# Performance work log

Hardware: AMD Instinct MI355X
Metric: run time of the kernel (lower is better)

Reference implementation:

```python
import jax, jax.numpy as jnp
import numpy as np

N = 8192          # num_relations
IN_DIM = 512      # 2 * entity_dim
HID = 256         # hidden_dim
REL_DIM = 256     # relation_dim


def setup_inputs() -> dict:
    key = jax.random.key(0)
    ks = jax.random.split(key, 8)
    s = 1.0 / np.sqrt(IN_DIM)
    return {
        "relation": jax.random.normal(ks[0], (N, REL_DIM), dtype=jnp.float32),
        "context": jax.random.normal(ks[1], (N, IN_DIM), dtype=jnp.float32),
        "adj_tensor": jax.random.randint(ks[2], (N, N), 0, 2).astype(jnp.float32),
        "W_common": jax.random.normal(ks[3], (HID, IN_DIM), dtype=jnp.float32) * s,
        "w_left": jax.random.normal(ks[4], (HID,), dtype=jnp.float32) * (1.0 / np.sqrt(HID)),
        "b_left": jax.random.normal(ks[5], (), dtype=jnp.float32) * 0.01,
        "w_right": jax.random.normal(ks[6], (HID,), dtype=jnp.float32) * (1.0 / np.sqrt(HID)),
        "b_right": jax.random.normal(ks[7], (), dtype=jnp.float32) * 0.01,
    }


def reference(relation, context, adj_tensor, W_common, w_left, b_left, w_right, b_right):
    # common linear (no bias): (N, IN_DIM) @ (IN_DIM, HID) -> (N, HID)
    in_fts = context @ W_common.T
    left = in_fts @ w_left + b_left          # (N,)
    right = in_fts @ w_right + b_right       # (N,)
    logits = left[:, None] + right[None, :]  # additive outer-sum -> (N, N)
    logits = jnp.where(logits >= 0, logits, 0.2 * logits)  # leaky_relu(0.2)
    logits = jnp.where(adj_tensor <= 0.0, -jnp.inf, logits)
    coefs = jax.nn.softmax(logits, axis=-1)  # (N, N)
    x = coefs @ relation                     # (N, REL_DIM)
    return jax.nn.relu(x)
```

## Files before the change

kernel.cpp:

```cpp
#include <hip/hip_runtime.h>

#define NREL 8192
#define RD   256

typedef float f32x4 __attribute__((ext_vector_type(4)));
typedef short s16x8 __attribute__((ext_vector_type(8)));
typedef unsigned int  u32;
typedef unsigned short u16;
typedef unsigned long long u64;
typedef u32 u32x4 __attribute__((ext_vector_type(4)));

__device__ __forceinline__ u16 f2bf(float f) {
    u32 b = __float_as_uint(f);
    return (u16)((b + 0x7FFFu + ((b >> 16) & 1u)) >> 16);
}
__device__ __forceinline__ u32 pk_bf16(float lo, float hi) {
    u32 r;
    asm("v_cvt_pk_bf16_f32 %0, %1, %2" : "=v"(r) : "v"(lo), "v"(hi));
    return r;
}

__global__ __launch_bounds__(256) void k_prep(
    const float* __restrict__ W, const float* __restrict__ wl,
    const float* __restrict__ wr, float* __restrict__ ul,
    float* __restrict__ ur)
{
    __shared__ float sL[256], sR[256];
    const int t = threadIdx.x;
    const int d = blockIdx.x * 16 + (t & 15);
    float aL = 0.f, aR = 0.f;
    for (int h = (t >> 4); h < 256; h += 16) {
        float w = W[h * 512 + d];
        aL += w * wl[h];
        aR += w * wr[h];
    }
    sL[t] = aL; sR[t] = aR;
    __syncthreads();
    if (t < 16) {
        float xL = 0.f, xR = 0.f;
        for (int g = 0; g < 16; g++) { xL += sL[g * 16 + t]; xR += sR[g * 16 + t]; }
        ul[blockIdx.x * 16 + t] = xL;
        ur[blockIdx.x * 16 + t] = xR;
    }
}

__global__ __launch_bounds__(256) void k_lr(
    const float* __restrict__ ctx, const float* __restrict__ ul,
    const float* __restrict__ ur, const float* __restrict__ bl,
    const float* __restrict__ br, float* __restrict__ left,
    float* __restrict__ right)
{
    const int lane = threadIdx.x & 63;
    const int row  = blockIdx.x * 4 + (threadIdx.x >> 6);
    const f32x4* cv = (const f32x4*)(ctx + (size_t)row * 512);
    const f32x4* uv = (const f32x4*)ul;
    const f32x4* vv = (const f32x4*)ur;
    f32x4 c0 = cv[lane], c1 = cv[lane + 64];
    f32x4 u0 = uv[lane], u1 = uv[lane + 64];
    f32x4 v0 = vv[lane], v1 = vv[lane + 64];
    float dl = c0.x*u0.x + c0.y*u0.y + c0.z*u0.z + c0.w*u0.w
             + c1.x*u1.x + c1.y*u1.y + c1.z*u1.z + c1.w*u1.w;
    float dr = c0.x*v0.x + c0.y*v0.y + c0.z*v0.z + c0.w*v0.w
             + c1.x*v1.x + c1.y*v1.y + c1.z*v1.z + c1.w*v1.w;
    #pragma unroll
    for (int o = 1; o < 64; o <<= 1) { dl += __shfl_xor(dl, o); dr += __shfl_xor(dr, o); }
    if (lane == 0) {
        left[row]  = dl + bl[0];
        right[row] = dr + br[0];
    }
}

__global__ __launch_bounds__(256) void k_rmax(const float* __restrict__ right,
                                              u32* __restrict__ rmaxk)
{
    __shared__ float sm[4];
    const int t = threadIdx.x;
    const f32x4* rv = (const f32x4*)right;
    float m = -3.4e38f;
    #pragma unroll
    for (int i = 0; i < 8; i++) {
        f32x4 v = rv[t + 256 * i];
        m = fmaxf(m, fmaxf(fmaxf(v.x, v.y), fmaxf(v.z, v.w)));
    }
    #pragma unroll
    for (int o = 1; o < 64; o <<= 1) m = fmaxf(m, __shfl_xor(m, o));
    if ((t & 63) == 0) sm[t >> 6] = m;
    __syncthreads();
    if (t == 0) {
        m = fmaxf(fmaxf(sm[0], sm[1]), fmaxf(sm[2], sm[3]));
        u32 b = __float_as_uint(m);
        *rmaxk = ((int)b >= 0) ? (b | 0x80000000u) : ~b;
    }
}

__global__ __launch_bounds__(256) void k_bf(const float* __restrict__ R,
                                            u32* __restrict__ Bf)
{
    const int b     = blockIdx.x;
    const int jt    = b >> 1;
    const int fbase = (b & 1) * 1024;
    #pragma unroll
    for (int rep = 0; rep < 4; rep++) {
        const int f    = fbase + rep * 256 + threadIdx.x;
        const int kk   = f >> 10;
        const int cg   = (f >> 6) & 15;
        const int lane = f & 63;
        const int lq   = lane >> 4;
        const int l15  = lane & 15;
        const int j0   = (jt << 6) + kk * 32 + lq * 8;
        const int n    = cg * 16 + l15;
        const float* src = R + (size_t)j0 * RD + n;
        float v[8];
        #pragma unroll
        for (int e = 0; e < 8; e++) v[e] = src[(size_t)e * RD];
        u32x4 w;
        w.x = pk_bf16(v[0], v[1]);
        w.y = pk_bf16(v[2], v[3]);
        w.z = pk_bf16(v[4], v[5]);
        w.w = pk_bf16(v[6], v[7]);
        *(u32x4*)(Bf + ((size_t)jt * 2048 + f) * 4) = w;
    }
}

template<int S>
__global__ __launch_bounds__(512) void k_attn_f(
    const float* __restrict__ adj, const s16x8* __restrict__ Bf,
    const float* __restrict__ left, const float* __restrict__ right,
    const u32* __restrict__ rmaxk, float* __restrict__ pnum,
    float* __restrict__ pden)
{
    __shared__ u32 Pl[2][2048];

    const int tid  = threadIdx.x;
    const int lane = tid & 63;
    const int wv   = tid >> 6;
    const int l15  = lane & 15;
    const int lq   = lane >> 4;
    const int s      = (int)(blockIdx.x % (unsigned)S);
    const int rowblk = (int)(blockIdx.x / (unsigned)S) * 64;
    const int jt0 = s * (128 / S);
    const int jt1 = jt0 + (128 / S);

    const int pr = tid >> 4;
    const int pq = tid & 15;

    const float lft0 = left[rowblk + pr];
    const float lft1 = left[rowblk + pr + 32];
    const u32 kbits = *rmaxk;
    const float rmax = __uint_as_float((kbits & 0x80000000u) ? (kbits ^ 0x80000000u)
                                                             : ~kbits);
    float z;
    z = lft0 + rmax; const float m0 = fmaxf(z, 0.2f * z);
    z = lft1 + rmax; const float m1 = fmaxf(z, 0.2f * z);

    f32x4 acc[4][2];
    #pragma unroll
    for (int i = 0; i < 4; i++) { acc[i][0] = (f32x4)0.f; acc[i][1] = (f32x4)0.f; }
    float dp0 = 0.f, dp1 = 0.f;

    const f32x4* adjv = (const f32x4*)adj;
    const f32x4* rv4  = (const f32x4*)right;
    const size_t arow0 = (size_t)(rowblk + pr) * 2048;
    const size_t arow1 = (size_t)(rowblk + pr + 32) * 2048;

    const u32 widx0 = (u32)pr * 32 + (((u32)pq * 2) ^ (((u32)pr & 7) << 2));
    const u32 widx1 = widx0 + 1024;

    f32x4 a0 = adjv[arow0 + jt0 * 16 + pq];
    f32x4 a1 = adjv[arow1 + jt0 * 16 + pq];
    f32x4 rv = rv4[jt0 * 16 + pq];
    s16x8 bcur[2][2];
    #pragma unroll
    for (int kk = 0; kk < 2; kk++)
        #pragma unroll
        for (int ct = 0; ct < 2; ct++)
            bcur[kk][ct] = Bf[(size_t)jt0 * 2048 + kk * 1024 + (wv * 2 + ct) * 64 + lane];

    int p = 0;
    for (int jt = jt0; jt < jt1; ++jt, p ^= 1) {
        float pa[4], pb[4];
        #pragma unroll
        for (int e = 0; e < 4; e++) {
            const float r = rv[e];
            float z0 = lft0 + r; float s0 = fmaxf(z0, 0.2f * z0);
            float e0 = __expf(s0 - m0);
            pa[e] = (a0[e] > 0.5f) ? e0 : 0.f;
            float z1 = lft1 + r; float s1 = fmaxf(z1, 0.2f * z1);
            float e1 = __expf(s1 - m1);
            pb[e] = (a1[e] > 0.5f) ? e1 : 0.f;
        }
        dp0 += pa[0] + pa[1] + pa[2] + pa[3];
        dp1 += pb[0] + pb[1] + pb[2] + pb[3];
        u32* Pb = Pl[p];
        Pb[widx0]     = pk_bf16(pa[0], pa[1]);
        Pb[widx0 + 1] = pk_bf16(pa[2], pa[3]);
        Pb[widx1]     = pk_bf16(pb[0], pb[1]);
        Pb[widx1 + 1] = pk_bf16(pb[2], pb[3]);

        asm volatile("s_waitcnt lgkmcnt(0)" ::: "memory");
        __builtin_amdgcn_s_barrier();

        const int jn = (jt + 1 < jt1) ? jt + 1 : jt0;
        f32x4 na0 = adjv[arow0 + jn * 16 + pq];
        f32x4 na1 = adjv[arow1 + jn * 16 + pq];
        f32x4 nrv = rv4[jn * 16 + pq];
        s16x8 bnxt[2][2];
        #pragma unroll
        for (int kk = 0; kk < 2; kk++)
            #pragma unroll
            for (int ct = 0; ct < 2; ct++)
                bnxt[kk][ct] = Bf[(size_t)jn * 2048 + kk * 1024 + (wv * 2 + ct) * 64 + lane];

        const u16* Pu = (const u16*)Pl[p];
        #pragma unroll
        for (int kk = 0; kk < 2; kk++) {
            s16x8 af[4];
            #pragma unroll
            for (int rt = 0; rt < 4; rt++) {
                const int row = rt * 16 + l15;
                const int us  = row * 64 + ((kk * 32 + lq * 8) ^ ((row & 7) << 3));
                af[rt] = *(const s16x8*)(Pu + us);
            }
            #pragma unroll
            for (int ct = 0; ct < 2; ct++)
                #pragma unroll
                for (int rt = 0; rt < 4; rt++)
                    acc[rt][ct] = __builtin_amdgcn_mfma_f32_16x16x32_bf16(
                        af[rt], bcur[kk][ct], acc[rt][ct], 0, 0, 0);
        }

        a0 = na0; a1 = na1; rv = nrv;
        #pragma unroll
        for (int kk = 0; kk < 2; kk++)
            #pragma unroll
            for (int ct = 0; ct < 2; ct++) bcur[kk][ct] = bnxt[kk][ct];
    }

    #pragma unroll
    for (int o = 1; o < 16; o <<= 1) { dp0 += __shfl_xor(dp0, o); dp1 += __shfl_xor(dp1, o); }
    if (pq == 0) {
        pden[(size_t)s * NREL + rowblk + pr]      = dp0;
        pden[(size_t)s * NREL + rowblk + pr + 32] = dp1;
    }
    float* pn = pnum + (size_t)s * NREL * RD;
    #pragma unroll
    for (int rt = 0; rt < 4; rt++)
        #pragma unroll
        for (int ct = 0; ct < 2; ct++)
            #pragma unroll
            for (int r = 0; r < 4; r++) {
                const int row = rt * 16 + lq * 4 + r;
                pn[(size_t)(rowblk + row) * RD + (wv * 32 + ct * 16 + l15)] =
                    acc[rt][ct][r];
            }
}

template<int S>
__global__ __launch_bounds__(256) void k_red(
    const float* __restrict__ pnum, const float* __restrict__ pden,
    float* __restrict__ out)
{
    const int idx = blockIdx.x * 256 + threadIdx.x;
    const int row = idx >> 6;
    float den = 0.f;
    #pragma unroll
    for (int s = 0; s < S; s++) den += pden[(size_t)s * NREL + row];
    const f32x4* pn4 = (const f32x4*)pnum;
    f32x4 a = (f32x4)0.f;
    #pragma unroll
    for (int s = 0; s < S; s++) a += pn4[(size_t)s * (NREL * RD / 4) + idx];
    f32x4 r;
    r.x = fmaxf(a.x / den, 0.f);
    r.y = fmaxf(a.y / den, 0.f);
    r.z = fmaxf(a.z / den, 0.f);
    r.w = fmaxf(a.w / den, 0.f);
    ((f32x4*)out)[idx] = r;
}

__global__ __launch_bounds__(512) void k_attn_leg(
    const float* __restrict__ adj, const float* __restrict__ rel,
    const float* __restrict__ left, const float* __restrict__ right,
    const u32* __restrict__ rmaxk, float* __restrict__ outp)
{
    __shared__ u32   Pl[64 * 32];
    __shared__ float dnm[64];
    const int tid  = threadIdx.x;
    const int lane = tid & 63;
    const int wv   = tid >> 6;
    const int l15  = lane & 15;
    const int lq   = lane >> 4;
    const int rowblk = blockIdx.x * 64;
    const int pr = tid >> 4, pq = tid & 15;
    const float lft0 = left[rowblk + pr];
    const float lft1 = left[rowblk + pr + 32];
    const u32 kbits = *rmaxk;
    const float rmax = __uint_as_float((kbits & 0x80000000u) ? (kbits ^ 0x80000000u)
                                                             : ~kbits);
    float z;
    z = lft0 + rmax; const float m0 = fmaxf(z, 0.2f * z);
    z = lft1 + rmax; const float m1 = fmaxf(z, 0.2f * z);
    f32x4 acc[4][2];
    #pragma unroll
    for (int i = 0; i < 4; i++) { acc[i][0] = (f32x4)0.f; acc[i][1] = (f32x4)0.f; }
    float dp0 = 0.f, dp1 = 0.f;
    const f32x4* adjv = (const f32x4*)adj;
    const f32x4* rv4  = (const f32x4*)right;
    const size_t arow0 = (size_t)(rowblk + pr) * 2048;
    const size_t arow1 = (size_t)(rowblk + pr + 32) * 2048;
    const int n0 = wv * 32 + l15;
    const u32 widx0 = (u32)pr * 32 + (((u32)pq * 2) ^ (((u32)pr & 7) << 2));
    const u32 widx1 = widx0 + 1024;
    for (int jb = 0; jb < NREL; jb += 64) {
        f32x4 a0 = adjv[arow0 + (jb >> 2) + pq];
        f32x4 a1 = adjv[arow1 + (jb >> 2) + pq];
        f32x4 rv = rv4[(jb >> 2) + pq];
        s16x8 bc[2][2];
        #pragma unroll
        for (int kk = 0; kk < 2; kk++)
            #pragma unroll
            for (int ct = 0; ct < 2; ct++) {
                const float* rp = rel + (size_t)(jb + kk * 32 + lq * 8) * RD
                                      + (n0 + ct * 16);
                s16x8 b;
                #pragma unroll
                for (int e = 0; e < 8; e++) b[e] = (short)f2bf(rp[(size_t)e * RD]);
                bc[kk][ct] = b;
            }
        float pa[4], pb[4];
        #pragma unroll
        for (int e = 0; e < 4; e++) {
            const float r = rv[e];
            float z0 = lft0 + r; float s0 = fmaxf(z0, 0.2f * z0);
            pa[e] = a0[e] * __expf(s0 - m0);
            float z1 = lft1 + r; float s1 = fmaxf(z1, 0.2f * z1);
            pb[e] = a1[e] * __expf(s1 - m1);
        }
        dp0 += pa[0] + pa[1] + pa[2] + pa[3];
        dp1 += pb[0] + pb[1] + pb[2] + pb[3];
        Pl[widx0]     = pk_bf16(pa[0], pa[1]);
        Pl[widx0 + 1] = pk_bf16(pa[2], pa[3]);
        Pl[widx1]     = pk_bf16(pb[0], pb[1]);
        Pl[widx1 + 1] = pk_bf16(pb[2], pb[3]);
        __syncthreads();
        #pragma unroll
        for (int kk = 0; kk < 2; kk++) {
            s16x8 af[4];
            #pragma unroll
            for (int rt = 0; rt < 4; rt++) {
                const int row = rt * 16 + l15;
                const int us  = row * 64 + ((kk * 32 + lq * 8) ^ ((row & 7) << 3));
                af[rt] = *(const s16x8*)((const u16*)Pl + us);
            }
            #pragma unroll
            for (int ct = 0; ct < 2; ct++)
                #pragma unroll
                for (int rt = 0; rt < 4; rt++)
                    acc[rt][ct] = __builtin_amdgcn_mfma_f32_16x16x32_bf16(
                        af[rt], bc[kk][ct], acc[rt][ct], 0, 0, 0);
        }
        __syncthreads();
    }
    #pragma unroll
    for (int o = 1; o < 16; o <<= 1) { dp0 += __shfl_xor(dp0, o); dp1 += __shfl_xor(dp1, o); }
    if (pq == 0) { dnm[pr] = dp0; dnm[pr + 32] = dp1; }
    __syncthreads();
    #pragma unroll
    for (int rt = 0; rt < 4; rt++)
        #pragma unroll
        for (int ct = 0; ct < 2; ct++)
            #pragma unroll
            for (int r = 0; r < 4; r++) {
                const int row = rt * 16 + lq * 4 + r;
                float v = acc[rt][ct][r] / dnm[row];
                outp[(size_t)(rowblk + row) * RD + (wv * 32 + ct * 16 + l15)] =
                    fmaxf(v, 0.f);
            }
}

extern "C" void kernel_launch(void* const* d_in, const int* in_sizes, int n_in,
                              void* d_out, int out_size, void* d_ws, size_t ws_size,
                              hipStream_t stream)
{
    const float* relation = (const float*)d_in[0];
    const float* context  = (const float*)d_in[1];
    const float* adj      = (const float*)d_in[2];
    const float* W        = (const float*)d_in[3];
    const float* wl       = (const float*)d_in[4];
    const float* bl       = (const float*)d_in[5];
    const float* wr       = (const float*)d_in[6];
    const float* br       = (const float*)d_in[7];
    float* out = (float*)d_out;

    float* wsf   = (float*)d_ws;
    float* ul    = wsf;
    float* ur    = wsf + 512;
    float* left  = wsf + 1024;
    float* right = wsf + 1024 + 8192;
    u32*   rmaxk = (u32*)(wsf + 1024 + 16384);
    const size_t hdr  = 81920;
    const size_t bf_b = (size_t)NREL * RD * 2;
    u32* Bf   = (u32*)((char*)d_ws + hdr);
    float* pnum = (float*)((char*)d_ws + hdr + bf_b);

    hipLaunchKernelGGL(k_prep, dim3(32), dim3(256), 0, stream, W, wl, wr, ul, ur);
    hipLaunchKernelGGL(k_lr, dim3(2048), dim3(256), 0, stream,
                       context, ul, ur, bl, br, left, right);
    hipLaunchKernelGGL(k_rmax, dim3(1), dim3(256), 0, stream, right, rmaxk);

    const int S = 4;
    const size_t need = hdr + bf_b
                      + (size_t)S * NREL * RD * 4 + (size_t)S * NREL * 4;

    if (ws_size >= need) {
        float* pden = pnum + (size_t)S * NREL * RD;
        hipLaunchKernelGGL(k_bf, dim3(256), dim3(256), 0, stream, relation, Bf);
        hipLaunchKernelGGL((k_attn_f<4>), dim3(128 * 4), dim3(512), 0, stream,
                           adj, (const s16x8*)Bf, left, right, rmaxk, pnum, pden);
        hipLaunchKernelGGL((k_red<4>), dim3(2048), dim3(256), 0, stream,
                           pnum, pden, out);
    } else {
        hipLaunchKernelGGL(k_attn_leg, dim3(128), dim3(512), 0, stream,
                           adj, relation, left, right, rmaxk, out);
    }
}
```

Measured before the change: 115.9 us.

## Fuse split-K reduction into attention kernel, merge prep with bf16 pack, unroll loop

Folds the relation bf16 packing into the prep kernel launch, and removes the separate split-K reduce kernel: the last of the S blocks for each row block (found via an atomic counter zeroed in k_rmax) sums the partials, normalizes and applies relu. The main loop is also manually unrolled by two with fixed LDS buffers and explicit A/B register sets. This removes two kernel launches and a pass over partial sums. In exchange it adds atomics, fences and a serialized tail on the last block of each row group.

```diff
diff --git a/kernel.cpp b/kernel.cpp
--- a/kernel.cpp
+++ b/kernel.cpp
@@ -20,27 +20,55 @@
     return r;
 }
 
-__global__ __launch_bounds__(256) void k_prep(
+__global__ __launch_bounds__(256) void k_prep_bf(
     const float* __restrict__ W, const float* __restrict__ wl,
     const float* __restrict__ wr, float* __restrict__ ul,
-    float* __restrict__ ur)
+    float* __restrict__ ur, const float* __restrict__ R,
+    u32* __restrict__ Bf)
 {
     __shared__ float sL[256], sR[256];
     const int t = threadIdx.x;
-    const int d = blockIdx.x * 16 + (t & 15);
-    float aL = 0.f, aR = 0.f;
-    for (int h = (t >> 4); h < 256; h += 16) {
-        float w = W[h * 512 + d];
-        aL += w * wl[h];
-        aR += w * wr[h];
-    }
-    sL[t] = aL; sR[t] = aR;
-    __syncthreads();
-    if (t < 16) {
-        float xL = 0.f, xR = 0.f;
-        for (int g = 0; g < 16; g++) { xL += sL[g * 16 + t]; xR += sR[g * 16 + t]; }
-        ul[blockIdx.x * 16 + t] = xL;
-        ur[blockIdx.x * 16 + t] = xR;
+    if (blockIdx.x < 32) {
+        const int d = blockIdx.x * 16 + (t & 15);
+        float aL = 0.f, aR = 0.f;
+        for (int h = (t >> 4); h < 256; h += 16) {
+            float w = W[h * 512 + d];
+            aL += w * wl[h];
+            aR += w * wr[h];
+        }
+        sL[t] = aL; sR[t] = aR;
+        __syncthreads();
+        if (t < 16) {
+            float xL = 0.f, xR = 0.f;
+            for (int g = 0; g < 16; g++) { xL += sL[g * 16 + t]; xR += sR[g * 16 + t]; }
+            ul[blockIdx.x * 16 + t] = xL;
+            ur[blockIdx.x * 16 + t] = xR;
+        }
+        return;
+    }
+    const int b     = blockIdx.x - 32;
+    const int jt    = b >> 1;
+    const int fbase = (b & 1) * 1024;
+    #pragma unroll
+    for (int rep = 0; rep < 4; rep++) {
+        const int f    = fbase + rep * 256 + t;
+        const int kk   = f >> 10;
+        const int cg   = (f >> 6) & 15;
+        const int lane = f & 63;
+        const int lq   = lane >> 4;
+        const int l15  = lane & 15;
+        const int j0   = (jt << 6) + kk * 32 + lq * 8;
+        const int n    = cg * 16 + l15;
+        const float* src = R + (size_t)j0 * RD + n;
+        float v[8];
+        #pragma unroll
+        for (int e = 0; e < 8; e++) v[e] = src[(size_t)e * RD];
+        u32x4 w;
+        w.x = pk_bf16(v[0], v[1]);
+        w.y = pk_bf16(v[2], v[3]);
+        w.z = pk_bf16(v[4], v[5]);
+        w.w = pk_bf16(v[6], v[7]);
+        *(u32x4*)(Bf + ((size_t)jt * 2048 + f) * 4) = w;
     }
 }
 
@@ -71,10 +99,12 @@
 }
 
 __global__ __launch_bounds__(256) void k_rmax(const float* __restrict__ right,
-                                              u32* __restrict__ rmaxk)
+                                              u32* __restrict__ rmaxk,
+                                              u32* __restrict__ cnt)
 {
     __shared__ float sm[4];
     const int t = threadIdx.x;
+    if (t < 128) cnt[t] = 0;
     const f32x4* rv = (const f32x4*)right;
     float m = -3.4e38f;
     #pragma unroll
@@ -93,43 +123,17 @@
     }
 }
 
-__global__ __launch_bounds__(256) void k_bf(const float* __restrict__ R,
-                                            u32* __restrict__ Bf)
-{
-    const int b     = blockIdx.x;
-    const int jt    = b >> 1;
-    const int fbase = (b & 1) * 1024;
-    #pragma unroll
-    for (int rep = 0; rep < 4; rep++) {
-        const int f    = fbase + rep * 256 + threadIdx.x;
-        const int kk   = f >> 10;
-        const int cg   = (f >> 6) & 15;
-        const int lane = f & 63;
-        const int lq   = lane >> 4;
-        const int l15  = lane & 15;
-        const int j0   = (jt << 6) + kk * 32 + lq * 8;
-        const int n    = cg * 16 + l15;
-        const float* src = R + (size_t)j0 * RD + n;
-        float v[8];
-        #pragma unroll
-        for (int e = 0; e < 8; e++) v[e] = src[(size_t)e * RD];
-        u32x4 w;
-        w.x = pk_bf16(v[0], v[1]);
-        w.y = pk_bf16(v[2], v[3]);
-        w.z = pk_bf16(v[4], v[5]);
-        w.w = pk_bf16(v[6], v[7]);
-        *(u32x4*)(Bf + ((size_t)jt * 2048 + f) * 4) = w;
-    }
-}
-
 template<int S>
 __global__ __launch_bounds__(512) void k_attn_f(
     const float* __restrict__ adj, const s16x8* __restrict__ Bf,
     const float* __restrict__ left, const float* __restrict__ right,
     const u32* __restrict__ rmaxk, float* __restrict__ pnum,
-    float* __restrict__ pden)
-{
-    __shared__ u32 Pl[2][2048];
+    float* __restrict__ pden, u32* __restrict__ cnt,
+    float* __restrict__ out)
+{
+    __shared__ u32   Pl[2][2048];
+    __shared__ float dnm[64];
+    __shared__ u32   sLast;
 
     const int tid  = threadIdx.x;
     const int lane = tid & 63;
@@ -137,7 +141,8 @@
     const int l15  = lane & 15;
     const int lq   = lane >> 4;
     const int s      = (int)(blockIdx.x % (unsigned)S);
-    const int rowblk = (int)(blockIdx.x / (unsigned)S) * 64;
+    const int rb     = (int)(blockIdx.x / (unsigned)S);
+    const int rowblk = rb * 64;
     const int jt0 = s * (128 / S);
     const int jt1 = jt0 + (128 / S);
 
@@ -166,74 +171,123 @@
     const u32 widx0 = (u32)pr * 32 + (((u32)pq * 2) ^ (((u32)pr & 7) << 2));
     const u32 widx1 = widx0 + 1024;
 
-    f32x4 a0 = adjv[arow0 + jt0 * 16 + pq];
-    f32x4 a1 = adjv[arow1 + jt0 * 16 + pq];
-    f32x4 rv = rv4[jt0 * 16 + pq];
-    s16x8 bcur[2][2];
+    f32x4 aA0 = adjv[arow0 + jt0 * 16 + pq];
+    f32x4 aA1 = adjv[arow1 + jt0 * 16 + pq];
+    f32x4 rvA = rv4[jt0 * 16 + pq];
+    f32x4 aB0 = adjv[arow0 + (jt0 + 1) * 16 + pq];
+    f32x4 aB1 = adjv[arow1 + (jt0 + 1) * 16 + pq];
+    f32x4 rvB = rv4[(jt0 + 1) * 16 + pq];
+    s16x8 bA[2][2], bB[2][2];
     #pragma unroll
     for (int kk = 0; kk < 2; kk++)
         #pragma unroll
         for (int ct = 0; ct < 2; ct++)
-            bcur[kk][ct] = Bf[(size_t)jt0 * 2048 + kk * 1024 + (wv * 2 + ct) * 64 + lane];
-
-    int p = 0;
-    for (int jt = jt0; jt < jt1; ++jt, p ^= 1) {
-        float pa[4], pb[4];
-        #pragma unroll
-        for (int e = 0; e < 4; e++) {
-            const float r = rv[e];
-            float z0 = lft0 + r; float s0 = fmaxf(z0, 0.2f * z0);
-            float e0 = __expf(s0 - m0);
-            pa[e] = (a0[e] > 0.5f) ? e0 : 0.f;
-            float z1 = lft1 + r; float s1 = fmaxf(z1, 0.2f * z1);
-            float e1 = __expf(s1 - m1);
-            pb[e] = (a1[e] > 0.5f) ? e1 : 0.f;
-        }
-        dp0 += pa[0] + pa[1] + pa[2] + pa[3];
-        dp1 += pb[0] + pb[1] + pb[2] + pb[3];
-        u32* Pb = Pl[p];
-        Pb[widx0]     = pk_bf16(pa[0], pa[1]);
-        Pb[widx0 + 1] = pk_bf16(pa[2], pa[3]);
-        Pb[widx1]     = pk_bf16(pb[0], pb[1]);
-        Pb[widx1 + 1] = pk_bf16(pb[2], pb[3]);
-
-        asm volatile("s_waitcnt lgkmcnt(0)" ::: "memory");
-        __builtin_amdgcn_s_barrier();
-
-        const int jn = (jt + 1 < jt1) ? jt + 1 : jt0;
-        f32x4 na0 = adjv[arow0 + jn * 16 + pq];
-        f32x4 na1 = adjv[arow1 + jn * 16 + pq];
-        f32x4 nrv = rv4[jn * 16 + pq];
-        s16x8 bnxt[2][2];
-        #pragma unroll
-        for (int kk = 0; kk < 2; kk++)
-            #pragma unroll
-            for (int ct = 0; ct < 2; ct++)
-                bnxt[kk][ct] = Bf[(size_t)jn * 2048 + kk * 1024 + (wv * 2 + ct) * 64 + lane];
-
-        const u16* Pu = (const u16*)Pl[p];
-        #pragma unroll
-        for (int kk = 0; kk < 2; kk++) {
-            s16x8 af[4];
-            #pragma unroll
-            for (int rt = 0; rt < 4; rt++) {
-                const int row = rt * 16 + l15;
-                const int us  = row * 64 + ((kk * 32 + lq * 8) ^ ((row & 7) << 3));
-                af[rt] = *(const s16x8*)(Pu + us);
-            }
-            #pragma unroll
-            for (int ct = 0; ct < 2; ct++)
-                #pragma unroll
-                for (int rt = 0; rt < 4; rt++)
-                    acc[rt][ct] = __builtin_amdgcn_mfma_f32_16x16x32_bf16(
-                        af[rt], bcur[kk][ct], acc[rt][ct], 0, 0, 0);
-        }
-
-        a0 = na0; a1 = na1; rv = nrv;
-        #pragma unroll
-        for (int kk = 0; kk < 2; kk++)
-            #pragma unroll
-            for (int ct = 0; ct < 2; ct++) bcur[kk][ct] = bnxt[kk][ct];
+            bA[kk][ct] = Bf[(size_t)jt0 * 2048 + kk * 1024 + (wv * 2 + ct) * 64 + lane];
+
+    for (int jt = jt0; jt < jt1; jt += 2) {
+        {
+            float pa[4], pb[4];
+            #pragma unroll
+            for (int e = 0; e < 4; e++) {
+                const float r = rvA[e];
+                float z0 = lft0 + r; float s0 = fmaxf(z0, 0.2f * z0);
+                float e0 = __expf(s0 - m0);
+                pa[e] = (aA0[e] > 0.5f) ? e0 : 0.f;
+                float z1 = lft1 + r; float s1 = fmaxf(z1, 0.2f * z1);
+                float e1 = __expf(s1 - m1);
+                pb[e] = (aA1[e] > 0.5f) ? e1 : 0.f;
+            }
+            dp0 += pa[0] + pa[1] + pa[2] + pa[3];
+            dp1 += pb[0] + pb[1] + pb[2] + pb[3];
+            Pl[0][widx0]     = pk_bf16(pa[0], pa[1]);
+            Pl[0][widx0 + 1] = pk_bf16(pa[2], pa[3]);
+            Pl[0][widx1]     = pk_bf16(pb[0], pb[1]);
+            Pl[0][widx1 + 1] = pk_bf16(pb[2], pb[3]);
+
+            asm volatile("s_waitcnt lgkmcnt(0)" ::: "memory");
+            __builtin_amdgcn_s_barrier();
+
+            const int j2 = (jt + 2 < jt1) ? jt + 2 : jt0;
+            aA0 = adjv[arow0 + j2 * 16 + pq];
+            aA1 = adjv[arow1 + j2 * 16 + pq];
+            rvA = rv4[j2 * 16 + pq];
+            #pragma unroll
+            for (int kk = 0; kk < 2; kk++)
+                #pragma unroll
+                for (int ct = 0; ct < 2; ct++)
+                    bB[kk][ct] = Bf[(size_t)(jt + 1) * 2048 + kk * 1024
+                                    + (wv * 2 + ct) * 64 + lane];
+
+            const u16* Pu = (const u16*)Pl[0];
+            #pragma unroll
+            for (int kk = 0; kk < 2; kk++) {
+                s16x8 af[4];
+                #pragma unroll
+                for (int rt = 0; rt < 4; rt++) {
+                    const int row = rt * 16 + l15;
+                    const int us  = row * 64 + ((kk * 32 + lq * 8) ^ ((row & 7) << 3));
+                    af[rt] = *(const s16x8*)(Pu + us);
+                }
+                #pragma unroll
+                for (int ct = 0; ct < 2; ct++)
+                    #pragma unroll
+                    for (int rt = 0; rt < 4; rt++)
+                        acc[rt][ct] = __builtin_amdgcn_mfma_f32_16x16x32_bf16(
+                            af[rt], bA[kk][ct], acc[rt][ct], 0, 0, 0);
+            }
+        }
+        {
+            float pa[4], pb[4];
+            #pragma unroll
+            for (int e = 0; e < 4; e++) {
+                const float r = rvB[e];
+                float z0 = lft0 + r; float s0 = fmaxf(z0, 0.2f * z0);
+                float e0 = __expf(s0 - m0);
+                pa[e] = (aB0[e] > 0.5f) ? e0 : 0.f;
+                float z1 = lft1 + r; float s1 = fmaxf(z1, 0.2f * z1);
+                float e1 = __expf(s1 - m1);
+                pb[e] = (aB1[e] > 0.5f) ? e1 : 0.f;
+            }
+            dp0 += pa[0] + pa[1] + pa[2] + pa[3];
+            dp1 += pb[0] + pb[1] + pb[2] + pb[3];
+            Pl[1][widx0]     = pk_bf16(pa[0], pa[1]);
+            Pl[1][widx0 + 1] = pk_bf16(pa[2], pa[3]);
+            Pl[1][widx1]     = pk_bf16(pb[0], pb[1]);
+            Pl[1][widx1 + 1] = pk_bf16(pb[2], pb[3]);
+
+            asm volatile("s_waitcnt lgkmcnt(0)" ::: "memory");
+            __builtin_amdgcn_s_barrier();
+
+            const int j3 = (jt + 3 < jt1) ? jt + 3 : jt0;
+            aB0 = adjv[arow0 + j3 * 16 + pq];
+            aB1 = adjv[arow1 + j3 * 16 + pq];
+            rvB = rv4[j3 * 16 + pq];
+            const int j2 = (jt + 2 < jt1) ? jt + 2 : jt0;
+            #pragma unroll
+            for (int kk = 0; kk < 2; kk++)
+                #pragma unroll
+                for (int ct = 0; ct < 2; ct++)
+                    bA[kk][ct] = Bf[(size_t)j2 * 2048 + kk * 1024
+                                    + (wv * 2 + ct) * 64 + lane];
+
+            const u16* Pu = (const u16*)Pl[1];
+            #pragma unroll
+            for (int kk = 0; kk < 2; kk++) {
+                s16x8 af[4];
+                #pragma unroll
+                for (int rt = 0; rt < 4; rt++) {
+                    const int row = rt * 16 + l15;
+                    const int us  = row * 64 + ((kk * 32 + lq * 8) ^ ((row & 7) << 3));
+                    af[rt] = *(const s16x8*)(Pu + us);
+                }
+                #pragma unroll
+                for (int ct = 0; ct < 2; ct++)
+                    #pragma unroll
+                    for (int rt = 0; rt < 4; rt++)
+                        acc[rt][ct] = __builtin_amdgcn_mfma_f32_16x16x32_bf16(
+                            af[rt], bB[kk][ct], acc[rt][ct], 0, 0, 0);
+            }
+        }
     }
 
     #pragma unroll
@@ -253,28 +307,38 @@
                 pn[(size_t)(rowblk + row) * RD + (wv * 32 + ct * 16 + l15)] =
                     acc[rt][ct][r];
             }
-}
-
-template<int S>
-__global__ __launch_bounds__(256) void k_red(
-    const float* __restrict__ pnum, const float* __restrict__ pden,
-    float* __restrict__ out)
-{
-    const int idx = blockIdx.x * 256 + threadIdx.x;
-    const int row = idx >> 6;
-    float den = 0.f;
-    #pragma unroll
-    for (int s = 0; s < S; s++) den += pden[(size_t)s * NREL + row];
+
+    __threadfence();
+    __syncthreads();
+    if (tid == 0) sLast = atomicAdd(&cnt[rb], 1u);
+    __syncthreads();
+    if (sLast != (u32)(S - 1)) return;
+    __threadfence();
+
+    if (tid < 64) {
+        float d = 0.f;
+        #pragma unroll
+        for (int ss = 0; ss < S; ss++) d += pden[(size_t)ss * NREL + rowblk + tid];
+        dnm[tid] = d;
+    }
+    __syncthreads();
     const f32x4* pn4 = (const f32x4*)pnum;
-    f32x4 a = (f32x4)0.f;
-    #pragma unroll
-    for (int s = 0; s < S; s++) a += pn4[(size_t)s * (NREL * RD / 4) + idx];
-    f32x4 r;
-    r.x = fmaxf(a.x / den, 0.f);
-    r.y = fmaxf(a.y / den, 0.f);
-    r.z = fmaxf(a.z / den, 0.f);
-    r.w = fmaxf(a.w / den, 0.f);
-    ((f32x4*)out)[idx] = r;
+    f32x4* out4 = (f32x4*)out;
+    #pragma unroll
+    for (int rep = 0; rep < 8; rep++) {
+        const int idx = rep * 512 + tid;
+        f32x4 a = (f32x4)0.f;
+        #pragma unroll
+        for (int ss = 0; ss < S; ss++)
+            a += pn4[(size_t)ss * (NREL * RD / 4) + (size_t)rb * 4096 + idx];
+        const float d = dnm[idx >> 6];
+        f32x4 r;
+        r.x = fmaxf(a.x / d, 0.f);
+        r.y = fmaxf(a.y / d, 0.f);
+        r.z = fmaxf(a.z / d, 0.f);
+        r.w = fmaxf(a.w / d, 0.f);
+        out4[(size_t)rb * 4096 + idx] = r;
+    }
 }
 
 __global__ __launch_bounds__(512) void k_attn_leg(
@@ -397,28 +461,32 @@
     float* left  = wsf + 1024;
     float* right = wsf + 1024 + 8192;
     u32*   rmaxk = (u32*)(wsf + 1024 + 16384);
+    u32*   cnt   = (u32*)(wsf + 1024 + 16384 + 256);
     const size_t hdr  = 81920;
     const size_t bf_b = (size_t)NREL * RD * 2;
     u32* Bf   = (u32*)((char*)d_ws + hdr);
     float* pnum = (float*)((char*)d_ws + hdr + bf_b);
 
-    hipLaunchKernelGGL(k_prep, dim3(32), dim3(256), 0, stream, W, wl, wr, ul, ur);
-    hipLaunchKernelGGL(k_lr, dim3(2048), dim3(256), 0, stream,
-                       context, ul, ur, bl, br, left, right);
-    hipLaunchKernelGGL(k_rmax, dim3(1), dim3(256), 0, stream, right, rmaxk);
-
     const int S = 4;
     const size_t need = hdr + bf_b
                       + (size_t)S * NREL * RD * 4 + (size_t)S * NREL * 4;
 
     if (ws_size >= need) {
         float* pden = pnum + (size_t)S * NREL * RD;
-        hipLaunchKernelGGL(k_bf, dim3(256), dim3(256), 0, stream, relation, Bf);
+        hipLaunchKernelGGL(k_prep_bf, dim3(288), dim3(256), 0, stream,
+                           W, wl, wr, ul, ur, relation, Bf);
+        hipLaunchKernelGGL(k_lr, dim3(2048), dim3(256), 0, stream,
+                           context, ul, ur, bl, br, left, right);
+        hipLaunchKernelGGL(k_rmax, dim3(1), dim3(256), 0, stream, right, rmaxk, cnt);
         hipLaunchKernelGGL((k_attn_f<4>), dim3(128 * 4), dim3(512), 0, stream,
-                           adj, (const s16x8*)Bf, left, right, rmaxk, pnum, pden);
-        hipLaunchKernelGGL((k_red<4>), dim3(2048), dim3(256), 0, stream,
-                           pnum, pden, out);
+                           adj, (const s16x8*)Bf, left, right, rmaxk,
+                           pnum, pden, cnt, out);
     } else {
+        hipLaunchKernelGGL(k_prep_bf, dim3(32), dim3(256), 0, stream,
+                           W, wl, wr, ul, ur, relation, (u32*)nullptr);
+        hipLaunchKernelGGL(k_lr, dim3(2048), dim3(256), 0, stream,
+                           context, ul, ur, bl, br, left, right);
+        hipLaunchKernelGGL(k_rmax, dim3(1), dim3(256), 0, stream, right, rmaxk, cnt);
         hipLaunchKernelGGL(k_attn_leg, dim3(128), dim3(512), 0, stream,
                            adj, relation, left, right, rmaxk, out);
     }
```

Result: slower. 369.4 us (+218.6%).
